# Optimization experiments

Hardware: AMD Instinct MI355X
Metric: run time of the kernel (lower is better)

## Reference

```python
import jax, jax.numpy as jnp
import numpy as np

C_S = 1024
C_Z = 128
H = 16
D = C_S // H  # 64
INF = 1000000.0


def _layernorm(x, g, b, eps=1e-5):
    mu = jnp.mean(x, axis=-1, keepdims=True)
    var = jnp.mean((x - mu) ** 2, axis=-1, keepdims=True)
    return (x - mu) * jax.lax.rsqrt(var + eps) * g + b


def setup_inputs() -> dict:
    key = jax.random.key(0)
    ks = jax.random.split(key, 12)
    B, N = 2, 512
    s = jax.random.normal(ks[0], (B, N, C_S), dtype=jnp.float32)
    z = jax.random.normal(ks[1], (B, N, N, C_Z), dtype=jnp.float32)
    mask = jnp.ones((B, N), dtype=jnp.float32)
    k_in = jax.random.normal(ks[2], (B, N, C_S), dtype=jnp.float32)
    sc = 1.0 / np.sqrt(C_S)
    wq = jax.random.normal(ks[3], (C_S, C_S), dtype=jnp.float32) * sc
    bq = jnp.zeros((C_S,), dtype=jnp.float32)
    wk = jax.random.normal(ks[4], (C_S, C_S), dtype=jnp.float32) * sc
    wv = jax.random.normal(ks[5], (C_S, C_S), dtype=jnp.float32) * sc
    wg = jax.random.normal(ks[6], (C_S, C_S), dtype=jnp.float32) * sc
    ln_g = jnp.ones((C_Z,), dtype=jnp.float32)
    ln_b = jnp.zeros((C_Z,), dtype=jnp.float32)
    wz = jax.random.normal(ks[7], (C_Z, H), dtype=jnp.float32) * (1.0 / np.sqrt(C_Z))
    # proj_o is zero-initialized in the original (final_init_); use small random
    # weights so the reference produces non-trivial outputs/gradients.
    wo = jax.random.normal(ks[8], (C_S, C_S), dtype=jnp.float32) * sc * 0.02
    return {"s": s, "z": z, "mask": mask, "k_in": k_in,
            "wq": wq, "bq": bq, "wk": wk, "wv": wv, "wg": wg,
            "ln_g": ln_g, "ln_b": ln_b, "wz": wz, "wo": wo,
            "multiplicity": 1}


def reference(s, z, mask, k_in, wq, bq, wk, wv, wg, ln_g, ln_b, wz, wo, multiplicity):
    B, N, _ = s.shape
    q = (jnp.dot(s, wq) + bq).reshape(B, N, H, D)
    k = jnp.dot(k_in, wk).reshape(B, N, H, D)
    v = jnp.dot(k_in, wv).reshape(B, N, H, D)
    # pair bias: LayerNorm(z) -> Linear(c_z -> H) -> (B, H, N, N)
    bias = jnp.dot(_layernorm(z, ln_g, ln_b), wz)  # (B, N, N, H)
    bias = jnp.transpose(bias, (0, 3, 1, 2))       # (B, H, N, N)
    bias = jnp.repeat(bias, multiplicity, axis=0)
    g = jax.nn.sigmoid(jnp.dot(s, wg))             # (B, N, c_s)
    # fp32 attention
    attn = jnp.einsum('bihd,bjhd->bhij', q, k) / np.sqrt(D).astype(np.float32)
    attn = attn + bias
    attn = attn + (1.0 - mask[:, None, None, :]) * (-INF)
    attn = jax.nn.softmax(attn, axis=-1)
    o = jnp.einsum('bhij,bjhd->bihd', attn, v).reshape(B, N, C_S)
    return jnp.dot(g * o, wo)
```

## Files before the change

### kernel.cpp

```cpp
#include <hip/hip_runtime.h>


typedef _Float16 h8 __attribute__((ext_vector_type(8)));
typedef _Float16 h4 __attribute__((ext_vector_type(4)));
typedef float f32x4 __attribute__((ext_vector_type(4)));
typedef unsigned int u32;

#define MFMA16(a, b, c) __builtin_amdgcn_mfma_f32_16x16x32_f16(a, b, c, 0, 0, 0)

__device__ __forceinline__ u32 pkrtz(float a, float b) {
  return __builtin_bit_cast(u32, __builtin_amdgcn_cvt_pkrtz(a, b));
}

__device__ __forceinline__ void gl_lds16(const void* g, void* l) {
  __builtin_amdgcn_global_load_lds(
      (const __attribute__((address_space(1))) u32*)g,
      (__attribute__((address_space(3))) u32*)l, 16, 0, 0);
}

static constexpr size_t OFF_S16   = 0;
static constexpr size_t OFF_KIN16 = 2097152;
static constexpr size_t OFF_WQT   = 4194304;
static constexpr size_t OFF_WKT   = 6291456;
static constexpr size_t OFF_WVT   = 8388608;
static constexpr size_t OFF_WGT   = 10485760;
static constexpr size_t OFF_WOT   = 12582912;
static constexpr size_t OFF_Q16   = 14680064;
static constexpr size_t OFF_K16   = 16777216;
static constexpr size_t OFF_V16   = 18874368;
static constexpr size_t OFF_VT16  = 20971520;
static constexpr size_t OFF_X16   = 23068672;
static constexpr size_t OFF_G32   = 25165824;
static constexpr size_t OFF_GWT   = 29360128;
static constexpr size_t OFF_GBW   = 29368320;
static constexpr size_t OFF_BIAS  = 33554432;

__global__ __launch_bounds__(256) void prep_kernel(
    const float* __restrict__ s, const float* __restrict__ kin,
    _Float16* __restrict__ s16, _Float16* __restrict__ kin16,
    const float* __restrict__ w0, const float* __restrict__ w1,
    const float* __restrict__ w2, const float* __restrict__ w3,
    const float* __restrict__ w4,
    _Float16* __restrict__ o0, _Float16* __restrict__ o1,
    _Float16* __restrict__ o2, _Float16* __restrict__ o3,
    _Float16* __restrict__ o4,
    const float* __restrict__ lng, const float* __restrict__ lnb,
    const float* __restrict__ wz, _Float16* __restrict__ gwT,
    float* __restrict__ Gbw) {
  int bid = blockIdx.x, t = threadIdx.x;
  if (bid < 1024) {
    const float* in = (bid < 512) ? s : kin;
    _Float16* out = (bid < 512) ? s16 : kin16;
    int i = (bid & 511) * 256 + t;
    const float4* p = (const float4*)in + (size_t)i * 2;
    float4 a = p[0], b = p[1];
    h8 v;
    v[0] = (_Float16)a.x; v[1] = (_Float16)a.y; v[2] = (_Float16)a.z; v[3] = (_Float16)a.w;
    v[4] = (_Float16)b.x; v[5] = (_Float16)b.y; v[6] = (_Float16)b.z; v[7] = (_Float16)b.w;
    *(h8*)(out + (size_t)i * 8) = v;
    return;
  }
  if (bid == 2304) {
    __shared__ float red[2][16][16];
    int h = t & 15, cg = t >> 4;
    float pg = 0.f, pb = 0.f;
#pragma unroll
    for (int u = 0; u < 8; ++u) {
      int c = cg * 8 + u;
      float w = wz[c * 16 + h];
      _Float16 gh = (_Float16)(lng[c] * w);
      gwT[h * 128 + c] = gh;
      pg += (float)gh;
      pb += lnb[c] * w;
    }
    red[0][h][cg] = pg; red[1][h][cg] = pb;
    __syncthreads();
    if (t < 32) {
      int hh = t & 15, which = t >> 4;
      float ssum = 0.f;
#pragma unroll
      for (int u = 0; u < 16; ++u) ssum += red[which][hh][u];
      Gbw[which * 16 + hh] = ssum;
    }
    return;
  }
  int r5 = bid - 1024;
  int y = r5 >> 8, tile = r5 & 255;
  const float* w; _Float16* o;
  switch (y) {
    case 0: w = w0; o = o0; break;
    case 1: w = w1; o = o1; break;
    case 2: w = w2; o = o2; break;
    case 3: w = w3; o = o3; break;
    default: w = w4; o = o4; break;
  }
  int tr = tile >> 4, tc = tile & 15;
  __shared__ _Float16 ts[64][72];
#pragma unroll
  for (int p = 0; p < 4; ++p) {
    int e = p * 1024 + t * 4;
    int r = e >> 6, c = e & 63;
    float4 v = *(const float4*)(w + (size_t)(tr * 64 + r) * 1024 + tc * 64 + c);
    h4 hv;
    hv[0] = (_Float16)v.x; hv[1] = (_Float16)v.y; hv[2] = (_Float16)v.z; hv[3] = (_Float16)v.w;
    *(h4*)&ts[r][c] = hv;
  }
  __syncthreads();
#pragma unroll
  for (int p = 0; p < 4; ++p) {
    int e = p * 1024 + t * 4;
    int n = e >> 6, k = e & 63;
    h4 hv;
#pragma unroll
    for (int u = 0; u < 4; ++u) hv[u] = ts[k + u][n];
    *(h4*)(o + (size_t)(tc * 64 + n) * 1024 + tr * 64 + k) = hv;
  }
}

__global__ __launch_bounds__(256) void ln_bias_kernel(
    const float* __restrict__ z, const _Float16* __restrict__ gwT,
    const float* __restrict__ Gbw, _Float16* __restrict__ bias16) {
  int jc = blockIdx.x, i = blockIdx.y, b = blockIdx.z;
  __shared__ float outs[64][17];
  int t = threadIdx.x, wid = t >> 6, lane = t & 63;
  int lr = lane & 15, hi = lane >> 4;
  const float* zr = z + (((size_t)b * 512 + i) * 512 + (size_t)jc * 64 + wid * 16 + lr) * 128;
  h8 af[4];
  float s1 = 0.f, s2 = 0.f;
#pragma unroll
  for (int kk = 0; kk < 4; ++kk) {
    float4 v0 = *(const float4*)(zr + kk * 32 + hi * 8);
    float4 v1 = *(const float4*)(zr + kk * 32 + hi * 8 + 4);
    s1 += v0.x + v0.y + v0.z + v0.w + v1.x + v1.y + v1.z + v1.w;
    s2 += v0.x * v0.x + v0.y * v0.y + v0.z * v0.z + v0.w * v0.w +
          v1.x * v1.x + v1.y * v1.y + v1.z * v1.z + v1.w * v1.w;
    h8 a;
    a[0] = (_Float16)v0.x; a[1] = (_Float16)v0.y; a[2] = (_Float16)v0.z; a[3] = (_Float16)v0.w;
    a[4] = (_Float16)v1.x; a[5] = (_Float16)v1.y; a[6] = (_Float16)v1.z; a[7] = (_Float16)v1.w;
    af[kk] = a;
  }
  s1 += __shfl_xor(s1, 16, 64); s2 += __shfl_xor(s2, 16, 64);
  s1 += __shfl_xor(s1, 32, 64); s2 += __shfl_xor(s2, 32, 64);
  float mu = s1 * (1.0f / 128.0f);
  float var = s2 * (1.0f / 128.0f) - mu * mu;
  float rs = rsqrtf(var + 1e-5f);
  f32x4 acc = {};
#pragma unroll
  for (int kk = 0; kk < 4; ++kk) {
    h8 bf = *(const h8*)(gwT + lr * 128 + kk * 32 + hi * 8);
    acc = MFMA16(af[kk], bf, acc);
  }
  float Gl = Gbw[lr], bwl = Gbw[16 + lr];
#pragma unroll
  for (int r = 0; r < 4; ++r) {
    int src = hi * 4 + r;
    float mur = __shfl(mu, src, 64);
    float rsr = __shfl(rs, src, 64);
    outs[wid * 16 + src][lr] = rsr * (acc[r] - mur * Gl) + bwl;
  }
  __syncthreads();
  {
    int hh = t >> 4, j0w = (t & 15) * 4;
    h4 ov;
    ov[0] = (_Float16)outs[j0w + 0][hh]; ov[1] = (_Float16)outs[j0w + 1][hh];
    ov[2] = (_Float16)outs[j0w + 2][hh]; ov[3] = (_Float16)outs[j0w + 3][hh];
    *(h4*)(bias16 + (((size_t)(b * 16 + hh) * 512) + i) * 512 + (size_t)jc * 64 + j0w) = ov;
  }
}

__global__ __launch_bounds__(256) void gemm_fused(
    const _Float16* __restrict__ s16, const _Float16* __restrict__ kin16,
    const _Float16* __restrict__ wqT, const _Float16* __restrict__ wkT,
    const _Float16* __restrict__ wvT, const _Float16* __restrict__ wgT,
    const float* __restrict__ bq,
    _Float16* __restrict__ q16, _Float16* __restrict__ k16,
    _Float16* __restrict__ v16, float* __restrict__ g32) {
  int mode = blockIdx.y;
  const _Float16 *A, *BT;
  switch (mode) {
    case 0: A = s16;   BT = wqT; break;
    case 1: A = kin16; BT = wkT; break;
    case 2: A = kin16; BT = wvT; break;
    default: A = s16;  BT = wgT; break;
  }
  int bm = blockIdx.x >> 4, bn = blockIdx.x & 15;
  __shared__ _Float16 As[2][64 * 64];
  __shared__ _Float16 Bs[2][64 * 64];
  int t = threadIdx.x, wid = t >> 6, lane = t & 63;
  int wr = wid >> 1, wc = wid & 1, lr = lane & 15, hi = lane >> 4;
  const _Float16* Ab = A + (size_t)(bm * 64) * 1024;
  const _Float16* Bb = BT + (size_t)(bn * 64) * 1024;
  auto STAGE = [&](int kt, int buf) {
    int k0 = kt * 64;
#pragma unroll
    for (int p = 0; p < 2; ++p) {
      int q = (wid * 2 + p) * 64 + lane;
      int row = q >> 3, c16 = q & 7;
      int coff = (c16 * 16) ^ ((row & 7) << 4);
      gl_lds16(Ab + (size_t)row * 1024 + k0 + (coff >> 1),
               (char*)As[buf] + (wid * 2 + p) * 1024);
      gl_lds16(Bb + (size_t)row * 1024 + k0 + (coff >> 1),
               (char*)Bs[buf] + (wid * 2 + p) * 1024);
    }
  };
  f32x4 acc[2][2] = {};
  STAGE(0, 0);
  __syncthreads();
  for (int kt = 0; kt < 16; ++kt) {
    int buf = kt & 1;
    if (kt < 15) STAGE(kt + 1, buf ^ 1);
#pragma unroll
    for (int kk = 0; kk < 2; ++kk) {
      h8 af[2], bf[2];
#pragma unroll
      for (int mi = 0; mi < 2; ++mi) {
        int row = wr * 32 + mi * 16 + lr;
        af[mi] = *(const h8*)((char*)As[buf] + row * 128 + ((kk * 64 + hi * 16) ^ ((lr & 7) << 4)));
      }
#pragma unroll
      for (int ni = 0; ni < 2; ++ni) {
        int row = wc * 32 + ni * 16 + lr;
        bf[ni] = *(const h8*)((char*)Bs[buf] + row * 128 + ((kk * 64 + hi * 16) ^ ((lr & 7) << 4)));
      }
#pragma unroll
      for (int mi = 0; mi < 2; ++mi)
#pragma unroll
        for (int ni = 0; ni < 2; ++ni)
          acc[mi][ni] = MFMA16(af[mi], bf[ni], acc[mi][ni]);
    }
    __syncthreads();
  }
#pragma unroll
  for (int mi = 0; mi < 2; ++mi)
#pragma unroll
    for (int ni = 0; ni < 2; ++ni)
#pragma unroll
      for (int r = 0; r < 4; ++r) {
        int row = bm * 64 + wr * 32 + mi * 16 + hi * 4 + r;
        int col = bn * 64 + wc * 32 + ni * 16 + lr;
        float v = acc[mi][ni][r];
        size_t o = (size_t)row * 1024 + col;
        switch (mode) {
          case 0: q16[o] = (_Float16)((v + bq[col]) * 0.125f); break;
          case 1: k16[o] = (_Float16)v; break;
          case 2: v16[o] = (_Float16)v; break;
          default: g32[o] = 1.0f / (1.0f + __expf(-v)); break;
        }
      }
}

__global__ __launch_bounds__(256) void transpose_v_kernel(
    const _Float16* __restrict__ v16, _Float16* __restrict__ vT) {
  int jt = blockIdx.x, bh = blockIdx.y, b = bh >> 4, h = bh & 15;
  __shared__ _Float16 ts[64][72];
  int t = threadIdx.x;
  const _Float16* src = v16 + ((size_t)b * 512 + (size_t)jt * 64) * 1024 + h * 64;
#pragma unroll
  for (int p = 0; p < 2; ++p) {
    int r = p * 32 + (t >> 3), c = (t & 7) * 8;
    *(int4*)&ts[r][c ^ (((r >> 3) & 7) << 3)] = *(const int4*)(src + (size_t)r * 1024 + c);
  }
  __syncthreads();
#pragma unroll
  for (int p = 0; p < 2; ++p) {
    int d = p * 32 + (t >> 3), j0 = (t & 7) * 8;
    h8 v;
#pragma unroll
    for (int u = 0; u < 8; ++u) {
      int j = j0 + u;
      v[u] = ts[j][d ^ (((j >> 3) & 7) << 3)];
    }
    *(h8*)(vT + ((size_t)bh * 64 + d) * 512 + (size_t)jt * 64 + j0) = v;
  }
}

__global__ __launch_bounds__(256) void flash_kernel(
    const _Float16* __restrict__ q16, const _Float16* __restrict__ k16,
    const _Float16* __restrict__ vT, const _Float16* __restrict__ bias16,
    const float* __restrict__ mask, const float* __restrict__ g32,
    _Float16* __restrict__ x16) {
  int bh = blockIdx.y, b = bh >> 4, h = bh & 15;
  int i0 = blockIdx.x * 64;
  __shared__ _Float16 Kc[2][128 * 64];
  __shared__ _Float16 Bc[2][64 * 128];
  __shared__ float mk[2][128];
  int t = threadIdx.x, wid = t >> 6, lane = t & 63;
  int lr = lane & 15, hi = lane >> 4;

  const _Float16* qrow = q16 + ((size_t)(b * 512) + i0 + wid * 16 + lr) * 1024 + h * 64;
  h8 qf0 = *(const h8*)(qrow + hi * 8);
  h8 qf1 = *(const h8*)(qrow + 32 + hi * 8);

  auto STAGE1 = [&](int c, int buf) {
    int j0 = c * 128;
    const _Float16* kb = k16 + ((size_t)(b * 512) + j0) * 1024 + h * 64;
    const _Float16* bb = bias16 + ((size_t)bh * 512 + i0) * 512 + j0;
#pragma unroll
    for (int p = 0; p < 4; ++p) {
      int q = (wid * 4 + p) * 64 + lane;
      {
        int row = q >> 3, c16 = q & 7;
        int coff = (c16 * 16) ^ ((row & 7) << 4);
        gl_lds16(kb + (size_t)row * 1024 + (coff >> 1),
                 (char*)Kc[buf] + (wid * 4 + p) * 1024);
      }
      {
        int row = q >> 4, c16 = q & 15;
        int coff = (c16 * 16) ^ ((row & 7) << 4);
        gl_lds16(bb + (size_t)row * 512 + (coff >> 1),
                 (char*)Bc[buf] + (wid * 4 + p) * 1024);
      }
    }
    if (t < 128) mk[buf][t] = (1.0f - mask[b * 512 + j0 + t]) * -1000000.0f;
  };

  f32x4 acc[32];
  STAGE1(0, 0);
  __syncthreads();
#pragma unroll
  for (int c = 0; c < 4; ++c) {
    int buf = c & 1;
    if (c < 3) STAGE1(c + 1, buf ^ 1);
#pragma unroll
    for (int jtl = 0; jtl < 8; ++jtl) {
      int jt = c * 8 + jtl;
      int krow = jtl * 16 + lr;
      h8 kf0 = *(const h8*)((char*)Kc[buf] + krow * 128 + ((hi * 16) ^ ((lr & 7) << 4)));
      h8 kf1 = *(const h8*)((char*)Kc[buf] + krow * 128 + ((64 + hi * 16) ^ ((lr & 7) << 4)));
      int brow = wid * 16 + lr;
      h4 bv = *(const h4*)((char*)Bc[buf] + brow * 256 + ((jtl * 32 + hi * 8) ^ ((lr & 7) << 4)));
      f32x4 mt = *(const f32x4*)&mk[buf][jtl * 16 + hi * 4];
      f32x4 a;
      a[0] = (float)bv[0] + mt[0]; a[1] = (float)bv[1] + mt[1];
      a[2] = (float)bv[2] + mt[2]; a[3] = (float)bv[3] + mt[3];
      a = MFMA16(kf0, qf0, a);
      a = MFMA16(kf1, qf1, a);
      acc[jt] = a;
    }
    __syncthreads();
  }

  float m = -3.4e38f;
#pragma unroll
  for (int jt = 0; jt < 32; ++jt)
    m = fmaxf(m, fmaxf(fmaxf(acc[jt][0], acc[jt][1]), fmaxf(acc[jt][2], acc[jt][3])));
  m = fmaxf(m, __shfl_xor(m, 16, 64));
  m = fmaxf(m, __shfl_xor(m, 32, 64));
  float ssum = 0.f;
#pragma unroll
  for (int jt = 0; jt < 32; ++jt) {
#pragma unroll
    for (int r = 0; r < 4; ++r) {
      float e = __expf(acc[jt][r] - m);
      acc[jt][r] = e;
      ssum += e;
    }
  }
  ssum += __shfl_xor(ssum, 16, 64);
  ssum += __shfl_xor(ssum, 32, 64);
  float inv = 1.0f / ssum;
  u32 pk0[32], pk1[32];
#pragma unroll
  for (int jt = 0; jt < 32; ++jt) {
    pk0[jt] = pkrtz(acc[jt][0] * inv, acc[jt][1] * inv);
    pk1[jt] = pkrtz(acc[jt][2] * inv, acc[jt][3] * inv);
  }

  auto STAGE2 = [&](int c, int buf) {
    int j0 = c * 128;
    const _Float16* vb = vT + ((size_t)bh * 64) * 512 + j0;
#pragma unroll
    for (int p = 0; p < 4; ++p) {
      int q = (wid * 4 + p) * 64 + lane;
      int row = q >> 4, c16 = q & 15;
      int coff = (c16 * 16) ^ ((row & 7) << 4);
      gl_lds16(vb + (size_t)row * 512 + (coff >> 1),
               (char*)Kc[buf] + (wid * 4 + p) * 1024);
    }
  };
  f32x4 oacc[4] = {};
  STAGE2(0, 0);
  __syncthreads();
#pragma unroll
  for (int c = 0; c < 4; ++c) {
    int buf = c & 1;
    if (c < 3) STAGE2(c + 1, buf ^ 1);
#pragma unroll
    for (int ktl = 0; ktl < 4; ++ktl) {
      int kt = c * 4 + ktl;
      int la = lr + ((hi & 1) << 5);
      int lb = la + 16;
      u32 a0 = __shfl(pk0[2 * kt], la, 64);
      u32 a1 = __shfl(pk1[2 * kt], la, 64);
      u32 b0 = __shfl(pk0[2 * kt], lb, 64);
      u32 b1 = __shfl(pk1[2 * kt], lb, 64);
      u32 c0 = __shfl(pk0[2 * kt + 1], la, 64);
      u32 c1 = __shfl(pk1[2 * kt + 1], la, 64);
      u32 d0 = __shfl(pk0[2 * kt + 1], lb, 64);
      u32 d1 = __shfl(pk1[2 * kt + 1], lb, 64);
      bool x1 = hi >= 2;
      uint4 au;
      au.x = x1 ? c0 : a0;
      au.y = x1 ? c1 : a1;
      au.z = x1 ? d0 : b0;
      au.w = x1 ? d1 : b1;
      h8 paf = __builtin_bit_cast(h8, au);
#pragma unroll
      for (int nt = 0; nt < 4; ++nt) {
        int vrow = nt * 16 + lr;
        h8 vf = *(const h8*)((char*)Kc[buf] + vrow * 256 + ((ktl * 64 + hi * 16) ^ ((lr & 7) << 4)));
        oacc[nt] = MFMA16(paf, vf, oacc[nt]);
      }
    }
    __syncthreads();
  }

  const float* gb = g32 + ((size_t)(b * 512) + i0) * 1024 + h * 64;
  _Float16* xb = x16 + ((size_t)(b * 512) + i0) * 1024 + h * 64;
#pragma unroll
  for (int nt = 0; nt < 4; ++nt)
#pragma unroll
    for (int r = 0; r < 4; ++r) {
      int il = wid * 16 + hi * 4 + r, d = nt * 16 + lr;
      size_t off = (size_t)il * 1024 + d;
      xb[off] = (_Float16)(oacc[nt][r] * gb[off]);
    }
}

__global__ __launch_bounds__(256) void gemm_o_kernel(
    const _Float16* __restrict__ x16, const _Float16* __restrict__ woT,
    float* __restrict__ out32) {
  int bm = blockIdx.x >> 4, bn = blockIdx.x & 15;
  __shared__ _Float16 As[2][64 * 64];
  __shared__ _Float16 Bs[2][64 * 64];
  int t = threadIdx.x, wid = t >> 6, lane = t & 63;
  int wr = wid >> 1, wc = wid & 1, lr = lane & 15, hi = lane >> 4;
  const _Float16* Ab = x16 + (size_t)(bm * 64) * 1024;
  const _Float16* Bb = woT + (size_t)(bn * 64) * 1024;
  auto STAGE = [&](int kt, int buf) {
    int k0 = kt * 64;
#pragma unroll
    for (int p = 0; p < 2; ++p) {
      int q = (wid * 2 + p) * 64 + lane;
      int row = q >> 3, c16 = q & 7;
      int coff = (c16 * 16) ^ ((row & 7) << 4);
      gl_lds16(Ab + (size_t)row * 1024 + k0 + (coff >> 1),
               (char*)As[buf] + (wid * 2 + p) * 1024);
      gl_lds16(Bb + (size_t)row * 1024 + k0 + (coff >> 1),
               (char*)Bs[buf] + (wid * 2 + p) * 1024);
    }
  };
  f32x4 acc[2][2] = {};
  STAGE(0, 0);
  __syncthreads();
  for (int kt = 0; kt < 16; ++kt) {
    int buf = kt & 1;
    if (kt < 15) STAGE(kt + 1, buf ^ 1);
#pragma unroll
    for (int kk = 0; kk < 2; ++kk) {
      h8 af[2], bf[2];
#pragma unroll
      for (int mi = 0; mi < 2; ++mi) {
        int row = wr * 32 + mi * 16 + lr;
        af[mi] = *(const h8*)((char*)As[buf] + row * 128 + ((kk * 64 + hi * 16) ^ ((lr & 7) << 4)));
      }
#pragma unroll
      for (int ni = 0; ni < 2; ++ni) {
        int row = wc * 32 + ni * 16 + lr;
        bf[ni] = *(const h8*)((char*)Bs[buf] + row * 128 + ((kk * 64 + hi * 16) ^ ((lr & 7) << 4)));
      }
#pragma unroll
      for (int mi = 0; mi < 2; ++mi)
#pragma unroll
        for (int ni = 0; ni < 2; ++ni)
          acc[mi][ni] = MFMA16(af[mi], bf[ni], acc[mi][ni]);
    }
    __syncthreads();
  }
#pragma unroll
  for (int mi = 0; mi < 2; ++mi)
#pragma unroll
    for (int ni = 0; ni < 2; ++ni)
#pragma unroll
      for (int r = 0; r < 4; ++r) {
        int row = bm * 64 + wr * 32 + mi * 16 + hi * 4 + r;
        int col = bn * 64 + wc * 32 + ni * 16 + lr;
        out32[(size_t)row * 1024 + col] = acc[mi][ni][r];
      }
}

extern "C" void kernel_launch(void* const* d_in, const int* in_sizes, int n_in,
                              void* d_out, int out_size, void* d_ws, size_t ws_size,
                              hipStream_t stream) {
  const float* s    = (const float*)d_in[0];
  const float* z    = (const float*)d_in[1];
  const float* mask = (const float*)d_in[2];
  const float* kin  = (const float*)d_in[3];
  const float* wq   = (const float*)d_in[4];
  const float* bq   = (const float*)d_in[5];
  const float* wk   = (const float*)d_in[6];
  const float* wv   = (const float*)d_in[7];
  const float* wg   = (const float*)d_in[8];
  const float* lng  = (const float*)d_in[9];
  const float* lnb  = (const float*)d_in[10];
  const float* wz   = (const float*)d_in[11];
  const float* wo   = (const float*)d_in[12];
  float* out = (float*)d_out;

  char* ws = (char*)d_ws;
  _Float16* s16   = (_Float16*)(ws + OFF_S16);
  _Float16* kin16 = (_Float16*)(ws + OFF_KIN16);
  _Float16* wqT   = (_Float16*)(ws + OFF_WQT);
  _Float16* wkT   = (_Float16*)(ws + OFF_WKT);
  _Float16* wvT   = (_Float16*)(ws + OFF_WVT);
  _Float16* wgT   = (_Float16*)(ws + OFF_WGT);
  _Float16* woT   = (_Float16*)(ws + OFF_WOT);
  _Float16* q16   = (_Float16*)(ws + OFF_Q16);
  _Float16* k16   = (_Float16*)(ws + OFF_K16);
  _Float16* v16   = (_Float16*)(ws + OFF_V16);
  _Float16* vT16  = (_Float16*)(ws + OFF_VT16);
  _Float16* x16   = (_Float16*)(ws + OFF_X16);
  float* g32      = (float*)(ws + OFF_G32);
  _Float16* gwT   = (_Float16*)(ws + OFF_GWT);
  float* Gbw      = (float*)(ws + OFF_GBW);
  _Float16* bias16= (_Float16*)(ws + OFF_BIAS);

  prep_kernel<<<2305, 256, 0, stream>>>(s, kin, s16, kin16,
                                        wq, wk, wv, wg, wo,
                                        wqT, wkT, wvT, wgT, woT,
                                        lng, lnb, wz, gwT, Gbw);
  ln_bias_kernel<<<dim3(8, 512, 2), 256, 0, stream>>>(z, gwT, Gbw, bias16);
  gemm_fused<<<dim3(256, 4), 256, 0, stream>>>(s16, kin16, wqT, wkT, wvT, wgT,
                                               bq, q16, k16, v16, g32);
  transpose_v_kernel<<<dim3(8, 32), 256, 0, stream>>>(v16, vT16);
  flash_kernel<<<dim3(8, 32), 256, 0, stream>>>(q16, k16, vT16, bias16,
                                                mask, g32, x16);
  gemm_o_kernel<<<256, 256, 0, stream>>>(x16, woT, out);
}
```

Before: 120.6 us.

## Load bias/mask directly to registers in flash kernel; halve gemm_o N tile

The flash kernel stops staging the pair-bias tile and mask through LDS and reads them straight from global memory into registers. This frees LDS, and a launch_bounds min-blocks hint of 2 is added to raise occupancy. The output GEMM switches to 64x32 tiles with 512 blocks, so more of the CUs have work. The trade-off is uncoalesced, unpipelined global loads for the bias in the inner loop, and lower per-block reuse in the GEMM.

```diff
diff --git a/kernel.cpp b/kernel.cpp
--- a/kernel.cpp
+++ b/kernel.cpp
@@ -274,7 +274,7 @@
   }
 }
 
-__global__ __launch_bounds__(256) void flash_kernel(
+__global__ __launch_bounds__(256, 2) void flash_kernel(
     const _Float16* __restrict__ q16, const _Float16* __restrict__ k16,
     const _Float16* __restrict__ vT, const _Float16* __restrict__ bias16,
     const float* __restrict__ mask, const float* __restrict__ g32,
@@ -282,8 +282,6 @@
   int bh = blockIdx.y, b = bh >> 4, h = bh & 15;
   int i0 = blockIdx.x * 64;
   __shared__ _Float16 Kc[2][128 * 64];
-  __shared__ _Float16 Bc[2][64 * 128];
-  __shared__ float mk[2][128];
   int t = threadIdx.x, wid = t >> 6, lane = t & 63;
   int lr = lane & 15, hi = lane >> 4;
 
@@ -291,27 +289,20 @@
   h8 qf0 = *(const h8*)(qrow + hi * 8);
   h8 qf1 = *(const h8*)(qrow + 32 + hi * 8);
 
+  const _Float16* bbase = bias16 + ((size_t)bh * 512 + i0 + wid * 16 + lr) * 512 + hi * 4;
+  const float* mbase = mask + b * 512 + hi * 4;
+
   auto STAGE1 = [&](int c, int buf) {
     int j0 = c * 128;
     const _Float16* kb = k16 + ((size_t)(b * 512) + j0) * 1024 + h * 64;
-    const _Float16* bb = bias16 + ((size_t)bh * 512 + i0) * 512 + j0;
 #pragma unroll
     for (int p = 0; p < 4; ++p) {
       int q = (wid * 4 + p) * 64 + lane;
-      {
-        int row = q >> 3, c16 = q & 7;
-        int coff = (c16 * 16) ^ ((row & 7) << 4);
-        gl_lds16(kb + (size_t)row * 1024 + (coff >> 1),
-                 (char*)Kc[buf] + (wid * 4 + p) * 1024);
-      }
-      {
-        int row = q >> 4, c16 = q & 15;
-        int coff = (c16 * 16) ^ ((row & 7) << 4);
-        gl_lds16(bb + (size_t)row * 512 + (coff >> 1),
-                 (char*)Bc[buf] + (wid * 4 + p) * 1024);
-      }
-    }
-    if (t < 128) mk[buf][t] = (1.0f - mask[b * 512 + j0 + t]) * -1000000.0f;
+      int row = q >> 3, c16 = q & 7;
+      int coff = (c16 * 16) ^ ((row & 7) << 4);
+      gl_lds16(kb + (size_t)row * 1024 + (coff >> 1),
+               (char*)Kc[buf] + (wid * 4 + p) * 1024);
+    }
   };
 
   f32x4 acc[32];
@@ -327,12 +318,13 @@
       int krow = jtl * 16 + lr;
       h8 kf0 = *(const h8*)((char*)Kc[buf] + krow * 128 + ((hi * 16) ^ ((lr & 7) << 4)));
       h8 kf1 = *(const h8*)((char*)Kc[buf] + krow * 128 + ((64 + hi * 16) ^ ((lr & 7) << 4)));
-      int brow = wid * 16 + lr;
-      h4 bv = *(const h4*)((char*)Bc[buf] + brow * 256 + ((jtl * 32 + hi * 8) ^ ((lr & 7) << 4)));
-      f32x4 mt = *(const f32x4*)&mk[buf][jtl * 16 + hi * 4];
+      h4 bv = *(const h4*)(bbase + jt * 16);
+      float4 mv = *(const float4*)(mbase + jt * 16);
       f32x4 a;
-      a[0] = (float)bv[0] + mt[0]; a[1] = (float)bv[1] + mt[1];
-      a[2] = (float)bv[2] + mt[2]; a[3] = (float)bv[3] + mt[3];
+      a[0] = (float)bv[0] + (1.0f - mv.x) * -1000000.0f;
+      a[1] = (float)bv[1] + (1.0f - mv.y) * -1000000.0f;
+      a[2] = (float)bv[2] + (1.0f - mv.z) * -1000000.0f;
+      a[3] = (float)bv[3] + (1.0f - mv.w) * -1000000.0f;
       a = MFMA16(kf0, qf0, a);
       a = MFMA16(kf1, qf1, a);
       acc[jt] = a;
@@ -430,13 +422,13 @@
 __global__ __launch_bounds__(256) void gemm_o_kernel(
     const _Float16* __restrict__ x16, const _Float16* __restrict__ woT,
     float* __restrict__ out32) {
-  int bm = blockIdx.x >> 4, bn = blockIdx.x & 15;
+  int bm = blockIdx.x >> 5, bn = blockIdx.x & 31;
   __shared__ _Float16 As[2][64 * 64];
-  __shared__ _Float16 Bs[2][64 * 64];
+  __shared__ _Float16 Bs[2][32 * 64];
   int t = threadIdx.x, wid = t >> 6, lane = t & 63;
   int wr = wid >> 1, wc = wid & 1, lr = lane & 15, hi = lane >> 4;
   const _Float16* Ab = x16 + (size_t)(bm * 64) * 1024;
-  const _Float16* Bb = woT + (size_t)(bn * 64) * 1024;
+  const _Float16* Bb = woT + (size_t)(bn * 32) * 1024;
   auto STAGE = [&](int kt, int buf) {
     int k0 = kt * 64;
 #pragma unroll
@@ -446,11 +438,16 @@
       int coff = (c16 * 16) ^ ((row & 7) << 4);
       gl_lds16(Ab + (size_t)row * 1024 + k0 + (coff >> 1),
                (char*)As[buf] + (wid * 2 + p) * 1024);
+    }
+    {
+      int q = t;
+      int row = q >> 3, c16 = q & 7;
+      int coff = (c16 * 16) ^ ((row & 7) << 4);
       gl_lds16(Bb + (size_t)row * 1024 + k0 + (coff >> 1),
-               (char*)Bs[buf] + (wid * 2 + p) * 1024);
+               (char*)Bs[buf] + wid * 1024);
     }
   };
-  f32x4 acc[2][2] = {};
+  f32x4 acc[2] = {};
   STAGE(0, 0);
   __syncthreads();
   for (int kt = 0; kt < 16; ++kt) {
@@ -458,35 +455,30 @@
     if (kt < 15) STAGE(kt + 1, buf ^ 1);
 #pragma unroll
     for (int kk = 0; kk < 2; ++kk) {
-      h8 af[2], bf[2];
+      h8 af[2], bf;
 #pragma unroll
       for (int mi = 0; mi < 2; ++mi) {
         int row = wr * 32 + mi * 16 + lr;
         af[mi] = *(const h8*)((char*)As[buf] + row * 128 + ((kk * 64 + hi * 16) ^ ((lr & 7) << 4)));
       }
-#pragma unroll
-      for (int ni = 0; ni < 2; ++ni) {
-        int row = wc * 32 + ni * 16 + lr;
-        bf[ni] = *(const h8*)((char*)Bs[buf] + row * 128 + ((kk * 64 + hi * 16) ^ ((lr & 7) << 4)));
+      {
+        int row = wc * 16 + lr;
+        bf = *(const h8*)((char*)Bs[buf] + row * 128 + ((kk * 64 + hi * 16) ^ ((lr & 7) << 4)));
       }
 #pragma unroll
       for (int mi = 0; mi < 2; ++mi)
-#pragma unroll
-        for (int ni = 0; ni < 2; ++ni)
-          acc[mi][ni] = MFMA16(af[mi], bf[ni], acc[mi][ni]);
+        acc[mi] = MFMA16(af[mi], bf, acc[mi]);
     }
     __syncthreads();
   }
 #pragma unroll
   for (int mi = 0; mi < 2; ++mi)
 #pragma unroll
-    for (int ni = 0; ni < 2; ++ni)
-#pragma unroll
-      for (int r = 0; r < 4; ++r) {
-        int row = bm * 64 + wr * 32 + mi * 16 + hi * 4 + r;
-        int col = bn * 64 + wc * 32 + ni * 16 + lr;
-        out32[(size_t)row * 1024 + col] = acc[mi][ni][r];
-      }
+    for (int r = 0; r < 4; ++r) {
+      int row = bm * 64 + wr * 32 + mi * 16 + hi * 4 + r;
+      int col = bn * 32 + wc * 16 + lr;
+      out32[(size_t)row * 1024 + col] = acc[mi][r];
+    }
 }
 
 extern "C" void kernel_launch(void* const* d_in, const int* in_sizes, int n_in,
@@ -535,5 +527,5 @@
   transpose_v_kernel<<<dim3(8, 32), 256, 0, stream>>>(v16, vT16);
   flash_kernel<<<dim3(8, 32), 256, 0, stream>>>(q16, k16, vT16, bias16,
                                                 mask, g32, x16);
-  gemm_o_kernel<<<256, 256, 0, stream>>>(x16, woT, out);
-}
+  gemm_o_kernel<<<512, 256, 0, stream>>>(x16, woT, out);
+}
```

Result: no change. 120.2 us (-0.3%).
